# Kernel optimization log

Hardware: AMD Instinct MI355X
Metric: run time of the kernel (lower is better)

## Reference

```python
import jax, jax.numpy as jnp
import numpy as np
from jax import lax

NUM_HEADS = 8
EPS = 1e-12  # F.normalize default eps


def setup_inputs() -> dict:
    key = jax.random.key(0)
    k1, k2, k3, k4 = jax.random.split(key, 4)
    b, c, h, w, d = 2, 128, 48, 48, 48
    x = jax.random.normal(k1, (b, c, h, w, d), dtype=jnp.float32)
    qkv_w = jax.random.normal(k2, (3 * c, c), dtype=jnp.float32) * 0.05
    dw_w = jax.random.normal(k3, (3 * c, 1, 3, 3, 3), dtype=jnp.float32) * 0.05
    proj_w = jax.random.normal(k4, (c, c), dtype=jnp.float32) * 0.05
    temperature = jnp.ones((1, NUM_HEADS, 1, 1), dtype=jnp.float32)
    return {"x": x, "qkv_w": qkv_w, "dw_w": dw_w, "proj_w": proj_w,
            "temperature": temperature}


def _l2_normalize(t):
    # F.normalize(t, dim=-1): t / max(||t||_2, eps)
    n = jnp.sqrt(jnp.sum(t * t, axis=-1, keepdims=True))
    return t / jnp.maximum(n, EPS)


def reference(x, qkv_w, dw_w, proj_w, temperature):
    b, c, h, w, d = x.shape
    dh = c // NUM_HEADS
    N = h * w * d
    # 1x1x1 pointwise conv (c -> 3c), no bias: pure channel GEMM
    qkv = jnp.einsum('oc,bchwd->bohwd', qkv_w, x)
    # depthwise 3x3x3 conv, padding=1, groups=3c
    qkv = lax.conv_general_dilated(
        qkv, dw_w, window_strides=(1, 1, 1), padding=[(1, 1)] * 3,
        dimension_numbers=('NCDHW', 'OIDHW', 'NCDHW'),
        feature_group_count=3 * c)
    q, k, v = jnp.split(qkv, 3, axis=1)
    q = q.reshape(b, NUM_HEADS, dh, N)
    k = k.reshape(b, NUM_HEADS, dh, N)
    v = v.reshape(b, NUM_HEADS, dh, N)
    q = _l2_normalize(q)
    k = _l2_normalize(k)
    # transposed attention: [b,H,dh,dh] score matrix over channels
    attn = jnp.einsum('bhin,bhjn->bhij', q, k) * temperature
    attn = jax.nn.softmax(attn, axis=-1)
    out = jnp.einsum('bhij,bhjn->bhin', attn, v).reshape(b, c, h, w, d)
    # 1x1x1 projection (c -> c), no bias
    return jnp.einsum('oc,bchwd->bohwd', proj_w, out)
```

## Files before the change

### kernel.cpp

```cpp
#include <hip/hip_runtime.h>
#include <hip/hip_bf16.h>
#include <stdint.h>
#include <stddef.h>

#define NSP 110592
#define SD  48
#define SD2 2304
#define CIN 128
#define C3  384
#define NH  8
#define NB  2
#define NQ  84934656ull

typedef __hip_bfloat16 bf16;
typedef __bf16 bf16x8 __attribute__((ext_vector_type(8)));
typedef float  f32x4  __attribute__((ext_vector_type(4)));

#define WOFF_QKVW 0
#define WOFF_DWW  49152
#define WOFF_PROJ 59520
#define WOFF_TEMP 75904
#define WTOTAL    75912

__device__ __forceinline__ float ldb(const bf16* p){ return __bfloat162float(*p); }
__device__ __forceinline__ float b2f(uint16_t u){
    union { float f; uint32_t i; } x; x.i = (uint32_t)u << 16; return x.f;
}
__device__ __forceinline__ uint16_t f2b(float f){
    bf16 h = __float2bfloat16(f); return *(uint16_t*)&h;
}

__global__ void k_sniff(const uint16_t* __restrict__ x16, int* __restrict__ flag)
{
    int t = threadIdx.x; int cnt = 0;
    for (int i = 0; i < 16; ++i) {
        uint16_t b = x16[(size_t)(t * 16 + i) * 2];
        int e = (b >> 7) & 0xFF;
        if (e >= 100 && e <= 140) ++cnt;
    }
    for (int off = 32; off; off >>= 1) cnt += __shfl_down(cnt, off, 64);
    __shared__ int s[4];
    if ((t & 63) == 0) s[t >> 6] = cnt;
    __syncthreads();
    if (t == 0) *flag = (s[0] + s[1] + s[2] + s[3] < 2048) ? 1 : 0;
}

__global__ void k_cvtw(const void* __restrict__ qw, const void* __restrict__ dw,
                       const void* __restrict__ pw, const void* __restrict__ tw,
                       bf16* __restrict__ wbuf, const int* __restrict__ flagp)
{
    int f = *flagp;
    int idx = blockIdx.x * 256 + threadIdx.x;
    if (idx >= WTOTAL) return;
    const void* src; int off;
    if (idx < WOFF_DWW)      { src = qw; off = idx; }
    else if (idx < WOFF_PROJ){ src = dw; off = idx - WOFF_DWW; }
    else if (idx < WOFF_TEMP){ src = pw; off = idx - WOFF_PROJ; }
    else                     { src = tw; off = idx - WOFF_TEMP; }
    float v = f ? ((const float*)src)[off]
                : __bfloat162float(((const bf16*)src)[off]);
    wbuf[idx] = __float2bfloat16(v);
}

__global__ __launch_bounds__(256) void k_transpose(const void* __restrict__ xin,
                                                   bf16* __restrict__ xT,
                                                   const int* __restrict__ flagp)
{
    int f = *flagp;
    int b = blockIdx.y;
    size_t tid = (size_t)blockIdx.x * 256 + threadIdx.x;
    int c = (int)(tid & 127);
    size_t n8 = tid >> 7;
    size_t base = ((size_t)b * CIN + c) * NSP + n8 * 8;
    bf16 pv[8];
    if (f) {
        const float* src = (const float*)xin + base;
        float4 a = *(const float4*)src;
        float4 d = *(const float4*)(src + 4);
        pv[0] = __float2bfloat16(a.x); pv[1] = __float2bfloat16(a.y);
        pv[2] = __float2bfloat16(a.z); pv[3] = __float2bfloat16(a.w);
        pv[4] = __float2bfloat16(d.x); pv[5] = __float2bfloat16(d.y);
        pv[6] = __float2bfloat16(d.z); pv[7] = __float2bfloat16(d.w);
    } else {
        uint4 v = *(const uint4*)((const bf16*)xin + base);
        const bf16* q = (const bf16*)&v;
#pragma unroll
        for (int j = 0; j < 8; ++j) pv[j] = q[j];
    }
    bf16* dst = xT + ((size_t)b * NSP + n8 * 8) * CIN + c;
#pragma unroll
    for (int j = 0; j < 8; ++j) dst[(size_t)j * CIN] = pv[j];
}

__global__ __launch_bounds__(256) void k_gemm_bt(const bf16* __restrict__ A,
                                                 const bf16* __restrict__ BT,
                                                 void* __restrict__ Cout,
                                                 int Mtotal,
                                                 const int* __restrict__ flagp,
                                                 int mblocks)
{
    __shared__ __align__(16) bf16 lA[128 * CIN];
    __shared__ __align__(16) bf16 lB[128 * CIN];
    int b = blockIdx.z;
    int bx = blockIdx.x;
    int mb, nb;
    if (mblocks == 3) {
        int g = bx / 24, w = bx % 24;
        nb = g * 8 + (w & 7);
        mb = w >> 3;
    } else { mb = 0; nb = bx; }
    size_t nbase = (size_t)nb * 128;
    const bf16* gA = A + (size_t)mb * 128 * CIN;
    const bf16* gB = BT + ((size_t)b * NSP + nbase) * CIN;
    int t = threadIdx.x;
#pragma unroll
    for (int i = 0; i < 8; ++i) {
        int off = (i * 256 + t) * 8;
        *(uint4*)&lA[off] = *(const uint4*)&gA[off];
        *(uint4*)&lB[off] = *(const uint4*)&gB[off];
    }
    __syncthreads();

    int wave = t >> 6, lane = t & 63;
    int wm = (wave & 1) * 64, wn = (wave >> 1) * 64;
    int lr = lane & 15, lq = lane >> 4;
    f32x4 acc[4][4];
#pragma unroll
    for (int mi = 0; mi < 4; ++mi)
#pragma unroll
        for (int ni = 0; ni < 4; ++ni) acc[mi][ni] = (f32x4){0.f, 0.f, 0.f, 0.f};

#pragma unroll
    for (int ks = 0; ks < 4; ++ks) {
        int kof = ks * 32 + lq * 8;
        bf16x8 af[4], bfv[4];
#pragma unroll
        for (int mi = 0; mi < 4; ++mi)
            af[mi] = *(const bf16x8*)&lA[(wm + mi * 16 + lr) * CIN + kof];
#pragma unroll
        for (int ni = 0; ni < 4; ++ni)
            bfv[ni] = *(const bf16x8*)&lB[(wn + ni * 16 + lr) * CIN + kof];
#pragma unroll
        for (int mi = 0; mi < 4; ++mi)
#pragma unroll
            for (int ni = 0; ni < 4; ++ni)
                acc[mi][ni] = __builtin_amdgcn_mfma_f32_16x16x32_bf16(
                    af[mi], bfv[ni], acc[mi][ni], 0, 0, 0);
    }

    int f32o = flagp ? *flagp : 0;
    size_t cb = ((size_t)b * Mtotal + (size_t)mb * 128) * NSP + nbase;
    if (f32o) {
        float* Cb = (float*)Cout + cb;
#pragma unroll
        for (int mi = 0; mi < 4; ++mi)
#pragma unroll
            for (int ni = 0; ni < 4; ++ni)
#pragma unroll
                for (int r = 0; r < 4; ++r)
                    Cb[(size_t)(wm + mi * 16 + lq * 4 + r) * NSP + wn + ni * 16 + lr]
                        = acc[mi][ni][r];
    } else {
        bf16* Cb = (bf16*)Cout + cb;
#pragma unroll
        for (int mi = 0; mi < 4; ++mi)
#pragma unroll
            for (int ni = 0; ni < 4; ++ni)
#pragma unroll
                for (int r = 0; r < 4; ++r)
                    Cb[(size_t)(wm + mi * 16 + lq * 4 + r) * NSP + wn + ni * 16 + lr]
                        = __float2bfloat16(acc[mi][ni][r]);
    }
}

#define PLN 3200
__global__ __launch_bounds__(256) void k_dwconv(const bf16* __restrict__ qkv1,
                                                const bf16* __restrict__ dw,
                                                bf16* __restrict__ qkv2,
                                                float* __restrict__ sums)
{
    __shared__ __align__(16) bf16 lds[8 * PLN];
    __shared__ float red[4];
    int bc = blockIdx.x;
    int slab = blockIdx.y;
    int z0 = slab * 6;
    int ch = bc % C3;
    int t = threadIdx.x;
    const bf16* src = qkv1 + (size_t)bc * NSP;
    bf16* dst = qkv2 + (size_t)bc * NSP;

    float wgt[27];
#pragma unroll
    for (int i = 0; i < 27; ++i) wgt[i] = ldb(&dw[ch * 27 + i]);

#pragma unroll
    for (int i = 0; i < 13; ++i) {
        int idx = i * 256 + t;
        if (idx < 3200) *(uint4*)&lds[idx * 8] = (uint4){0, 0, 0, 0};
    }
    __syncthreads();

#pragma unroll
    for (int i = 0; i < 9; ++i) {
        int vidx = i * 256 + t;
        int p = vidx / 288;
        int r = vidx - p * 288;
        int y = r / 6;
        int dg = r - y * 6;
        int zp = z0 - 1 + p;
        if ((unsigned)zp < SD) {
            uint4 v = *(const uint4*)&src[(size_t)zp * SD2 + y * SD + dg * 8];
            *(uint4*)&lds[(p * PLN + (y + 1) * 64 + 8 + dg * 8)] = v;
        }
    }
    __syncthreads();

    float ssq = 0.f;
#pragma unroll 1
    for (int r = 0; r < 3; ++r) {
        int s = r * 256 + t;
        if (s < 576) {
            int y = s / 12;
            int c4 = (s - y * 12) * 4;
            float acc[6][4];
#pragma unroll
            for (int oz = 0; oz < 6; ++oz)
#pragma unroll
                for (int d = 0; d < 4; ++d) acc[oz][d] = 0.f;

#pragma unroll
            for (int pl = 0; pl < 8; ++pl) {
                const uint16_t* P =
                    (const uint16_t*)lds + pl * PLN + y * 64 + 8 + c4;
                float v[3][6];
#pragma unroll
                for (int dy = 0; dy < 3; ++dy) {
                    const uint16_t* R = P + dy * 64;
                    uint2 m = *(const uint2*)R;
                    v[dy][0] = b2f(R[-1]);
                    v[dy][1] = b2f((uint16_t)m.x);
                    v[dy][2] = b2f((uint16_t)(m.x >> 16));
                    v[dy][3] = b2f((uint16_t)m.y);
                    v[dy][4] = b2f((uint16_t)(m.y >> 16));
                    v[dy][5] = b2f(R[4]);
                }
                float p0[4] = {0.f,0.f,0.f,0.f};
                float p1[4] = {0.f,0.f,0.f,0.f};
                float p2[4] = {0.f,0.f,0.f,0.f};
#pragma unroll
                for (int dy = 0; dy < 3; ++dy)
#pragma unroll
                    for (int dd = 0; dd < 3; ++dd) {
                        float w0 = wgt[dy * 3 + dd];
                        float w1 = wgt[9 + dy * 3 + dd];
                        float w2 = wgt[18 + dy * 3 + dd];
#pragma unroll
                        for (int d = 0; d < 4; ++d) {
                            float xv = v[dy][d + dd];
                            if (pl <= 5)            p0[d] += w0 * xv;
                            if (pl >= 1 && pl <= 6) p1[d] += w1 * xv;
                            if (pl >= 2)            p2[d] += w2 * xv;
                        }
                    }
#pragma unroll
                for (int d = 0; d < 4; ++d) {
                    if (pl <= 5)            acc[pl][d]     += p0[d];
                    if (pl >= 1 && pl <= 6) acc[pl - 1][d] += p1[d];
                    if (pl >= 2)            acc[pl - 2][d] += p2[d];
                }
            }
#pragma unroll
            for (int oz = 0; oz < 6; ++oz) {
                uint16_t u0 = f2b(acc[oz][0]), u1 = f2b(acc[oz][1]);
                uint16_t u2 = f2b(acc[oz][2]), u3 = f2b(acc[oz][3]);
                uint2 o;
                o.x = (uint32_t)u0 | ((uint32_t)u1 << 16);
                o.y = (uint32_t)u2 | ((uint32_t)u3 << 16);
                *(uint2*)&dst[(size_t)(z0 + oz) * SD2 + y * SD + c4] = o;
#pragma unroll
                for (int d = 0; d < 4; ++d) ssq += acc[oz][d] * acc[oz][d];
            }
        }
    }

    for (int off = 32; off; off >>= 1) ssq += __shfl_down(ssq, off, 64);
    if ((t & 63) == 0) red[t >> 6] = ssq;
    __syncthreads();
    if (t == 0) atomicAdd(&sums[bc], red[0] + red[1] + red[2] + red[3]);
}

__global__ __launch_bounds__(256) void k_scores(const bf16* __restrict__ qkv2,
                                                float* __restrict__ scores)
{
    int b = blockIdx.z, h = blockIdx.y;
    const bf16* qb = qkv2 + ((size_t)b * C3 + h * 16) * NSP;
    const bf16* kb = qkv2 + ((size_t)b * C3 + 128 + h * 16) * NSP;
    int t = threadIdx.x, w = t >> 6, lane = t & 63;
    int m = lane & 15, q4 = lane >> 4;
    size_t n0 = (size_t)blockIdx.x * 1024 + (size_t)w * 256 + (size_t)q4 * 8;
    const bf16* qp = qb + (size_t)m * NSP + n0;
    const bf16* kp = kb + (size_t)m * NSP + n0;
    f32x4 acc = (f32x4){0.f, 0.f, 0.f, 0.f};
#pragma unroll
    for (int it = 0; it < 8; ++it) {
        bf16x8 a  = *(const bf16x8*)(qp + it * 32);
        bf16x8 bb = *(const bf16x8*)(kp + it * 32);
        acc = __builtin_amdgcn_mfma_f32_16x16x32_bf16(a, bb, acc, 0, 0, 0);
    }
    float* srow = scores + (size_t)(b * NH + h) * 256;
#pragma unroll
    for (int r = 0; r < 4; ++r)
        atomicAdd(&srow[(q4 * 4 + r) * 16 + m], acc[r]);
}

__global__ void k_softmax(const float* __restrict__ scores,
                          const float* __restrict__ sums,
                          const bf16* __restrict__ temp,
                          float* __restrict__ attn)
{
    int t = threadIdx.x;
    int h = (t >> 4) & 7, b = t >> 7;
    float tau = __bfloat162float(temp[h]);
    float invq = 1.f / fmaxf(sqrtf(sums[b * C3 + (t & 127)]), 1e-12f);
    const float* srow = scores + (size_t)t * 16;
    float s[16]; float mx = -3.4e38f;
#pragma unroll
    for (int j = 0; j < 16; ++j) {
        float invk = 1.f / fmaxf(sqrtf(sums[b * C3 + 128 + h * 16 + j]), 1e-12f);
        s[j] = srow[j] * invq * invk * tau;
        mx = fmaxf(mx, s[j]);
    }
    float sum = 0.f;
#pragma unroll
    for (int j = 0; j < 16; ++j) { s[j] = expf(s[j] - mx); sum += s[j]; }
    float inv = 1.f / sum;
    float* arow = attn + (size_t)t * 16;
#pragma unroll
    for (int j = 0; j < 16; ++j) arow[j] = s[j] * inv;
}

__global__ __launch_bounds__(256) void k_av(const bf16* __restrict__ qkv2,
                                            const float* __restrict__ attn,
                                            bf16* __restrict__ outT)
{
    int b = blockIdx.z, h = blockIdx.y;
    const bf16* vb = qkv2 + ((size_t)b * C3 + 256 + h * 16) * NSP;
    __shared__ float at[256];
    int t = threadIdx.x;
    {
        int i = t >> 4, j = t & 15;
        at[j * 16 + i] = attn[(size_t)(b * NH + h) * 256 + t];
    }
    __syncthreads();
    size_t n0 = (size_t)blockIdx.x * 1024 + (size_t)t * 4;
    float acc[16][4];
#pragma unroll
    for (int i = 0; i < 16; ++i)
#pragma unroll
        for (int k = 0; k < 4; ++k) acc[i][k] = 0.f;
#pragma unroll
    for (int j = 0; j < 16; ++j) {
        uint2 raw = *(const uint2*)&vb[(size_t)j * NSP + n0];
        const bf16* rp = (const bf16*)&raw;
        float vf[4];
#pragma unroll
        for (int k = 0; k < 4; ++k) vf[k] = ldb(&rp[k]);
#pragma unroll
        for (int i = 0; i < 16; ++i) {
            float wv = at[j * 16 + i];
#pragma unroll
            for (int k = 0; k < 4; ++k) acc[i][k] += wv * vf[k];
        }
    }
    bf16* ob = outT + ((size_t)b * NSP + n0) * CIN + h * 16;
#pragma unroll
    for (int k = 0; k < 4; ++k) {
        bf16 tmp[16];
#pragma unroll
        for (int i = 0; i < 16; ++i) tmp[i] = __float2bfloat16(acc[i][k]);
        *(uint4*)&ob[(size_t)k * CIN]     = *(uint4*)&tmp[0];
        *(uint4*)&ob[(size_t)k * CIN + 8] = *(uint4*)&tmp[8];
    }
}

extern "C" void kernel_launch(void* const* d_in, const int* in_sizes, int n_in,
                              void* d_out, int out_size, void* d_ws, size_t ws_size,
                              hipStream_t stream)
{
    const void *px = nullptr, *pq = nullptr, *pd = nullptr, *pp = nullptr, *pt = nullptr;
    for (int i = 0; i < n_in; ++i) {
        switch (in_sizes[i]) {
            case 28311552: px = d_in[i]; break;
            case 49152:    pq = d_in[i]; break;
            case 10368:    pd = d_in[i]; break;
            case 16384:    pp = d_in[i]; break;
            case 8:        pt = d_in[i]; break;
        }
    }
    const size_t required = NQ * 4 + (1u << 20);
    if (!px || !pq || !pd || !pp || !pt || ws_size < required) {
        (void)hipMemsetAsync(d_out, 0, (size_t)out_size * 2, stream);
        return;
    }

    char* ws = (char*)d_ws;
    bf16* qkv1 = (bf16*)ws;
    bf16* qkv2 = (bf16*)(ws + NQ * 2);
    char* small = ws + NQ * 4;
    int*   flag   = (int*)small;
    float* sums   = (float*)(small + 256);
    float* scores = (float*)(small + 8192);
    float* attn   = (float*)(small + 24576);
    bf16*  wbuf   = (bf16*)(small + 40960);
    bf16* xT   = qkv2;
    bf16* outT = qkv1;

    (void)hipMemsetAsync(small, 0, 40960, stream);
    k_sniff<<<1, 256, 0, stream>>>((const uint16_t*)px, flag);
    k_cvtw<<<(WTOTAL + 255) / 256, 256, 0, stream>>>(pq, pd, pp, pt, wbuf, flag);
    k_transpose<<<dim3(6912, NB), 256, 0, stream>>>(px, xT, flag);
    k_gemm_bt<<<dim3(864 * 3, 1, NB), 256, 0, stream>>>(
        wbuf + WOFF_QKVW, xT, qkv1, C3, nullptr, 3);
    k_dwconv<<<dim3(NB * C3, 8), 256, 0, stream>>>(qkv1, wbuf + WOFF_DWW, qkv2, sums);
    k_scores<<<dim3(108, NH, NB), 256, 0, stream>>>(qkv2, scores);
    k_softmax<<<1, 256, 0, stream>>>(scores, sums, wbuf + WOFF_TEMP, attn);
    k_av<<<dim3(108, NH, NB), 256, 0, stream>>>(qkv2, attn, outT);
    k_gemm_bt<<<dim3(864, 1, NB), 256, 0, stream>>>(
        wbuf + WOFF_PROJ, outT, d_out, CIN, flag, 1);
}
```

Before: 555.6 us.

## Register-block dwconv over two rows, and replace score atomics with per-block partials

```diff
diff --git a/kernel.cpp b/kernel.cpp
--- a/kernel.cpp
+++ b/kernel.cpp
@@ -173,7 +173,7 @@
     }
 }
 
-#define PLN 3200
+#define PLN 3000
 __global__ __launch_bounds__(256) void k_dwconv(const bf16* __restrict__ qkv1,
                                                 const bf16* __restrict__ dw,
                                                 bf16* __restrict__ qkv2,
@@ -194,9 +194,9 @@
     for (int i = 0; i < 27; ++i) wgt[i] = ldb(&dw[ch * 27 + i]);
 
 #pragma unroll
-    for (int i = 0; i < 13; ++i) {
+    for (int i = 0; i < 12; ++i) {
         int idx = i * 256 + t;
-        if (idx < 3200) *(uint4*)&lds[idx * 8] = (uint4){0, 0, 0, 0};
+        if (idx < 3000) *(uint4*)&lds[idx * 8] = (uint4){0, 0, 0, 0};
     }
     __syncthreads();
 
@@ -210,76 +210,88 @@
         int zp = z0 - 1 + p;
         if ((unsigned)zp < SD) {
             uint4 v = *(const uint4*)&src[(size_t)zp * SD2 + y * SD + dg * 8];
-            *(uint4*)&lds[(p * PLN + (y + 1) * 64 + 8 + dg * 8)] = v;
+            uint2* L = (uint2*)&lds[p * PLN + (y + 1) * 60 + 8 + dg * 8];
+            L[0] = (uint2){v.x, v.y};
+            L[1] = (uint2){v.z, v.w};
         }
     }
     __syncthreads();
 
     float ssq = 0.f;
 #pragma unroll 1
-    for (int r = 0; r < 3; ++r) {
+    for (int r = 0; r < 2; ++r) {
         int s = r * 256 + t;
-        if (s < 576) {
-            int y = s / 12;
-            int c4 = (s - y * 12) * 4;
-            float acc[6][4];
+        if (s < 288) {
+            int k = s % 12;
+            int yp = s / 12;
+            int y0 = yp * 2;
+            int c4 = k * 4;
+            float acc[6][2][4];
 #pragma unroll
             for (int oz = 0; oz < 6; ++oz)
 #pragma unroll
-                for (int d = 0; d < 4; ++d) acc[oz][d] = 0.f;
+                for (int h2 = 0; h2 < 2; ++h2)
+#pragma unroll
+                    for (int d = 0; d < 4; ++d) acc[oz][h2][d] = 0.f;
 
 #pragma unroll
             for (int pl = 0; pl < 8; ++pl) {
                 const uint16_t* P =
-                    (const uint16_t*)lds + pl * PLN + y * 64 + 8 + c4;
-                float v[3][6];
-#pragma unroll
-                for (int dy = 0; dy < 3; ++dy) {
-                    const uint16_t* R = P + dy * 64;
+                    (const uint16_t*)lds + pl * PLN + y0 * 60 + 8 + c4;
+                float v[4][6];
+#pragma unroll
+                for (int rr = 0; rr < 4; ++rr) {
+                    const uint16_t* R = P + rr * 60;
                     uint2 m = *(const uint2*)R;
-                    v[dy][0] = b2f(R[-1]);
-                    v[dy][1] = b2f((uint16_t)m.x);
-                    v[dy][2] = b2f((uint16_t)(m.x >> 16));
-                    v[dy][3] = b2f((uint16_t)m.y);
-                    v[dy][4] = b2f((uint16_t)(m.y >> 16));
-                    v[dy][5] = b2f(R[4]);
+                    v[rr][0] = b2f(R[-1]);
+                    v[rr][1] = b2f((uint16_t)m.x);
+                    v[rr][2] = b2f((uint16_t)(m.x >> 16));
+                    v[rr][3] = b2f((uint16_t)m.y);
+                    v[rr][4] = b2f((uint16_t)(m.y >> 16));
+                    v[rr][5] = b2f(R[4]);
                 }
-                float p0[4] = {0.f,0.f,0.f,0.f};
-                float p1[4] = {0.f,0.f,0.f,0.f};
-                float p2[4] = {0.f,0.f,0.f,0.f};
-#pragma unroll
-                for (int dy = 0; dy < 3; ++dy)
-#pragma unroll
-                    for (int dd = 0; dd < 3; ++dd) {
-                        float w0 = wgt[dy * 3 + dd];
-                        float w1 = wgt[9 + dy * 3 + dd];
-                        float w2 = wgt[18 + dy * 3 + dd];
-#pragma unroll
-                        for (int d = 0; d < 4; ++d) {
-                            float xv = v[dy][d + dd];
-                            if (pl <= 5)            p0[d] += w0 * xv;
-                            if (pl >= 1 && pl <= 6) p1[d] += w1 * xv;
-                            if (pl >= 2)            p2[d] += w2 * xv;
+#pragma unroll
+                for (int h2 = 0; h2 < 2; ++h2) {
+                    float p0[4] = {0.f,0.f,0.f,0.f};
+                    float p1[4] = {0.f,0.f,0.f,0.f};
+                    float p2[4] = {0.f,0.f,0.f,0.f};
+#pragma unroll
+                    for (int dy = 0; dy < 3; ++dy)
+#pragma unroll
+                        for (int dd = 0; dd < 3; ++dd) {
+                            float w0 = wgt[dy * 3 + dd];
+                            float w1 = wgt[9 + dy * 3 + dd];
+                            float w2 = wgt[18 + dy * 3 + dd];
+#pragma unroll
+                            for (int d = 0; d < 4; ++d) {
+                                float xv = v[h2 + dy][d + dd];
+                                if (pl <= 5)            p0[d] += w0 * xv;
+                                if (pl >= 1 && pl <= 6) p1[d] += w1 * xv;
+                                if (pl >= 2)            p2[d] += w2 * xv;
+                            }
                         }
+#pragma unroll
+                    for (int d = 0; d < 4; ++d) {
+                        if (pl <= 5)            acc[pl][h2][d]     += p0[d];
+                        if (pl >= 1 && pl <= 6) acc[pl - 1][h2][d] += p1[d];
+                        if (pl >= 2)            acc[pl - 2][h2][d] += p2[d];
                     }
-#pragma unroll
-                for (int d = 0; d < 4; ++d) {
-                    if (pl <= 5)            acc[pl][d]     += p0[d];
-                    if (pl >= 1 && pl <= 6) acc[pl - 1][d] += p1[d];
-                    if (pl >= 2)            acc[pl - 2][d] += p2[d];
                 }
             }
 #pragma unroll
-            for (int oz = 0; oz < 6; ++oz) {
-                uint16_t u0 = f2b(acc[oz][0]), u1 = f2b(acc[oz][1]);
-                uint16_t u2 = f2b(acc[oz][2]), u3 = f2b(acc[oz][3]);
-                uint2 o;
-                o.x = (uint32_t)u0 | ((uint32_t)u1 << 16);
-                o.y = (uint32_t)u2 | ((uint32_t)u3 << 16);
-                *(uint2*)&dst[(size_t)(z0 + oz) * SD2 + y * SD + c4] = o;
-#pragma unroll
-                for (int d = 0; d < 4; ++d) ssq += acc[oz][d] * acc[oz][d];
-            }
+            for (int oz = 0; oz < 6; ++oz)
+#pragma unroll
+                for (int h2 = 0; h2 < 2; ++h2) {
+                    uint16_t u0 = f2b(acc[oz][h2][0]), u1 = f2b(acc[oz][h2][1]);
+                    uint16_t u2 = f2b(acc[oz][h2][2]), u3 = f2b(acc[oz][h2][3]);
+                    uint2 o;
+                    o.x = (uint32_t)u0 | ((uint32_t)u1 << 16);
+                    o.y = (uint32_t)u2 | ((uint32_t)u3 << 16);
+                    *(uint2*)&dst[(size_t)(z0 + oz) * SD2 + (y0 + h2) * SD + c4] = o;
+#pragma unroll
+                    for (int d = 0; d < 4; ++d)
+                        ssq += acc[oz][h2][d] * acc[oz][h2][d];
+                }
         }
     }
 
@@ -290,44 +302,58 @@
 }
 
 __global__ __launch_bounds__(256) void k_scores(const bf16* __restrict__ qkv2,
-                                                float* __restrict__ scores)
-{
+                                                float* __restrict__ partials)
+{
+    __shared__ float lred[4][256];
     int b = blockIdx.z, h = blockIdx.y;
     const bf16* qb = qkv2 + ((size_t)b * C3 + h * 16) * NSP;
     const bf16* kb = qkv2 + ((size_t)b * C3 + 128 + h * 16) * NSP;
     int t = threadIdx.x, w = t >> 6, lane = t & 63;
     int m = lane & 15, q4 = lane >> 4;
-    size_t n0 = (size_t)blockIdx.x * 1024 + (size_t)w * 256 + (size_t)q4 * 8;
+    size_t n0 = (size_t)blockIdx.x * 4096 + (size_t)w * 1024 + (size_t)q4 * 8;
     const bf16* qp = qb + (size_t)m * NSP + n0;
     const bf16* kp = kb + (size_t)m * NSP + n0;
     f32x4 acc = (f32x4){0.f, 0.f, 0.f, 0.f};
 #pragma unroll
-    for (int it = 0; it < 8; ++it) {
+    for (int it = 0; it < 32; ++it) {
         bf16x8 a  = *(const bf16x8*)(qp + it * 32);
         bf16x8 bb = *(const bf16x8*)(kp + it * 32);
         acc = __builtin_amdgcn_mfma_f32_16x16x32_bf16(a, bb, acc, 0, 0, 0);
     }
-    float* srow = scores + (size_t)(b * NH + h) * 256;
 #pragma unroll
     for (int r = 0; r < 4; ++r)
-        atomicAdd(&srow[(q4 * 4 + r) * 16 + m], acc[r]);
-}
-
-__global__ void k_softmax(const float* __restrict__ scores,
+        lred[w][(q4 * 4 + r) * 16 + m] = acc[r];
+    __syncthreads();
+    float val = lred[0][t] + lred[1][t] + lred[2][t] + lred[3][t];
+    partials[((size_t)(b * NH + h) * 27 + blockIdx.x) * 256 + t] = val;
+}
+
+__global__ void k_softmax(const float* __restrict__ partials,
                           const float* __restrict__ sums,
                           const bf16* __restrict__ temp,
                           float* __restrict__ attn)
 {
     int t = threadIdx.x;
-    int h = (t >> 4) & 7, b = t >> 7;
+    int i = t & 15, h = (t >> 4) & 7, b = t >> 7;
     float tau = __bfloat162float(temp[h]);
     float invq = 1.f / fmaxf(sqrtf(sums[b * C3 + (t & 127)]), 1e-12f);
-    const float* srow = scores + (size_t)t * 16;
-    float s[16]; float mx = -3.4e38f;
+    const float* rp = partials + (size_t)(b * NH + h) * 27 * 256 + i * 16;
+    float s[16];
+#pragma unroll
+    for (int j = 0; j < 16; ++j) s[j] = 0.f;
+    for (int p = 0; p < 27; ++p) {
+#pragma unroll
+        for (int j = 0; j < 4; ++j) {
+            float4 v = *(const float4*)&rp[p * 256 + j * 4];
+            s[j * 4 + 0] += v.x; s[j * 4 + 1] += v.y;
+            s[j * 4 + 2] += v.z; s[j * 4 + 3] += v.w;
+        }
+    }
+    float mx = -3.4e38f;
 #pragma unroll
     for (int j = 0; j < 16; ++j) {
         float invk = 1.f / fmaxf(sqrtf(sums[b * C3 + 128 + h * 16 + j]), 1e-12f);
-        s[j] = srow[j] * invq * invk * tau;
+        s[j] = s[j] * invq * invk * tau;
         mx = fmaxf(mx, s[j]);
     }
     float sum = 0.f;
@@ -407,23 +433,23 @@
     bf16* qkv1 = (bf16*)ws;
     bf16* qkv2 = (bf16*)(ws + NQ * 2);
     char* small = ws + NQ * 4;
-    int*   flag   = (int*)small;
-    float* sums   = (float*)(small + 256);
-    float* scores = (float*)(small + 8192);
-    float* attn   = (float*)(small + 24576);
-    bf16*  wbuf   = (bf16*)(small + 40960);
+    int*   flag     = (int*)small;
+    float* sums     = (float*)(small + 256);
+    float* attn     = (float*)(small + 8192);
+    bf16*  wbuf     = (bf16*)(small + 24576);
+    float* partials = (float*)(small + 180224);
     bf16* xT   = qkv2;
     bf16* outT = qkv1;
 
-    (void)hipMemsetAsync(small, 0, 40960, stream);
+    (void)hipMemsetAsync(small, 0, 4096, stream);
     k_sniff<<<1, 256, 0, stream>>>((const uint16_t*)px, flag);
     k_cvtw<<<(WTOTAL + 255) / 256, 256, 0, stream>>>(pq, pd, pp, pt, wbuf, flag);
     k_transpose<<<dim3(6912, NB), 256, 0, stream>>>(px, xT, flag);
     k_gemm_bt<<<dim3(864 * 3, 1, NB), 256, 0, stream>>>(
         wbuf + WOFF_QKVW, xT, qkv1, C3, nullptr, 3);
     k_dwconv<<<dim3(NB * C3, 8), 256, 0, stream>>>(qkv1, wbuf + WOFF_DWW, qkv2, sums);
-    k_scores<<<dim3(108, NH, NB), 256, 0, stream>>>(qkv2, scores);
-    k_softmax<<<1, 256, 0, stream>>>(scores, sums, wbuf + WOFF_TEMP, attn);
+    k_scores<<<dim3(27, NH, NB), 256, 0, stream>>>(qkv2, partials);
+    k_softmax<<<1, 256, 0, stream>>>(partials, sums, wbuf + WOFF_TEMP, attn);
     k_av<<<dim3(108, NH, NB), 256, 0, stream>>>(qkv2, attn, outT);
     k_gemm_bt<<<dim3(864, 1, NB), 256, 0, stream>>>(
         wbuf + WOFF_PROJ, outT, d_out, CIN, flag, 1);
```

Result: no change. 566.2 us (+1.9%).
